# Performance work log

Hardware: AMD Instinct MI355X
Metric: run time of the kernel (lower is better)

Reference implementation:

```python
import jax, jax.numpy as jnp
import numpy as np

D_MODEL = 1024
N_HEADS = 16
D_HEAD = D_MODEL // N_HEADS
B, S = 2, 2048


def setup_inputs() -> dict:
    key = jax.random.key(0)
    ks = jax.random.split(key, 8)
    scale = 1.0 / np.sqrt(D_MODEL)
    return {
        "x": jax.random.normal(ks[0], (B, S, D_MODEL), dtype=jnp.float32),
        "Wq": jax.random.normal(ks[1], (D_MODEL, D_MODEL), dtype=jnp.float32) * scale,
        "bq": jnp.zeros((D_MODEL,), dtype=jnp.float32),
        "Wk": jax.random.normal(ks[2], (D_MODEL, D_MODEL), dtype=jnp.float32) * scale,
        "bk": jnp.zeros((D_MODEL,), dtype=jnp.float32),
        "Wv": jax.random.normal(ks[3], (D_MODEL, D_MODEL), dtype=jnp.float32) * scale,
        "bv": jnp.zeros((D_MODEL,), dtype=jnp.float32),
        "Wo": jax.random.normal(ks[4], (D_MODEL, D_MODEL), dtype=jnp.float32) * scale,
    }


def reference(x, Wq, bq, Wk, bk, Wv, bv, Wo):
    Bsz, Slen, D = x.shape
    # projections -> [B, H, S, Dh]
    def split_heads(t):
        return t.reshape(Bsz, Slen, N_HEADS, D_HEAD).transpose(0, 2, 1, 3)
    q = split_heads(x @ Wq + bq)
    k = split_heads(x @ Wk + bk)
    v = split_heads(x @ Wv + bv)
    scale = jnp.sqrt(jnp.float32(D_HEAD))
    scores = jnp.einsum('bhsd,bhtd->bhst', q, k) / scale  # [B,H,S,S]
    causal_mask = jnp.tril(jnp.ones((Slen, Slen), dtype=jnp.bool_))
    scores = jnp.where(causal_mask, scores, jnp.finfo(scores.dtype).min)
    attn = jax.nn.softmax(scores, axis=-1)
    # deterministic=True path: dropout is identity
    out = jnp.einsum('bhst,bhtd->bhsd', attn, v)
    out = out.transpose(0, 2, 1, 3).reshape(Bsz, Slen, D)
    return out @ Wo
```

## Files before the change

kernel.cpp:

```cpp
#include <hip/hip_runtime.h>
#include <hip/hip_bf16.h>

#define BATCH   2
#define SEQ     2048
#define DMODEL  1024
#define NHEADS  16
#define DHEAD   64
#define MROWS   (BATCH*SEQ)
#define NBH     (BATCH*NHEADS)

typedef float  f32x4  __attribute__((ext_vector_type(4)));
typedef short  s16x4  __attribute__((ext_vector_type(4)));
typedef short  s16x8  __attribute__((ext_vector_type(8)));
typedef __bf16 bf16x8 __attribute__((ext_vector_type(8)));

__device__ __forceinline__ short f2bf(float f) {
  union { float f; unsigned u; } v; v.f = f;
  return (short)((v.u + 0x7fffu + ((v.u >> 16) & 1u)) >> 16);
}
__device__ __forceinline__ float bf2f(short s) {
  union { unsigned u; float f; } v; v.u = ((unsigned)(unsigned short)s) << 16;
  return v.f;
}

__global__ void prep_fused(const float* __restrict__ x, short* __restrict__ xb,
                           const float* __restrict__ Wq, const float* __restrict__ Wk,
                           const float* __restrict__ Wv, const float* __restrict__ Wo,
                           short* __restrict__ WtQKV, short* __restrict__ WtO) {
  __shared__ float t[32][33];
  int z = blockIdx.z;
  int tx = threadIdx.x, ty = threadIdx.y;
  if (z >= 4) {
    int blk = (z - 4) * 1024 + blockIdx.y * 32 + blockIdx.x;
    int i = (blk * 256 + ty * 32 + tx) * 4;
    float4 v = *(const float4*)(x + i);
    s16x4 o = { f2bf(v.x), f2bf(v.y), f2bf(v.z), f2bf(v.w) };
    *(s16x4*)(xb + i) = o;
    return;
  }
  const float* W; short* Wt;
  if      (z == 0) { W = Wq; Wt = WtQKV; }
  else if (z == 1) { W = Wk; Wt = WtQKV + (1u << 20); }
  else if (z == 2) { W = Wv; Wt = WtQKV + (2u << 20); }
  else             { W = Wo; Wt = WtO; }
  int n0 = blockIdx.x * 32, k0 = blockIdx.y * 32;
  #pragma unroll
  for (int i = 0; i < 32; i += 8) t[ty + i][tx] = W[(k0 + ty + i) * DMODEL + n0 + tx];
  __syncthreads();
  #pragma unroll
  for (int i = 0; i < 32; i += 8) Wt[(n0 + ty + i) * DMODEL + k0 + tx] = f2bf(t[tx][ty + i]);
}

template<int MT, int NT, int EPI>
__global__ __launch_bounds__(256) void gemm_bf16(
    const short* __restrict__ A, const short* __restrict__ Bt,
    const float* __restrict__ bq, const float* __restrict__ bk, const float* __restrict__ bv,
    short* __restrict__ qb, short* __restrict__ kb, short* __restrict__ vt,
    float* __restrict__ out)
{
  constexpr int K = DMODEL, BK = 32;
  constexpr int WM = MT / 2, WN = NT / 2;
  constexpr int TM = WM / 16, TN = WN / 16;
  constexpr int CA = MT * BK / 512;
  constexpr int CB = NT * BK / 512;
  constexpr int SME = MT * BK + NT * BK;
  __shared__ short smem[SME];
  short* la = smem;
  short* lb = smem + MT * BK;
  const int tid = threadIdx.x;
  const int wave = tid >> 6, lane = tid & 63;
  const int quad = lane >> 4, l16 = lane & 15;
  const int wr = wave >> 1, wc = wave & 1;
  const int nx = gridDim.x, ny = gridDim.y;
  const int g = blockIdx.y * nx + blockIdx.x;
  const int xcd = g & 7, rr = g >> 3;
  const int m0 = (xcd * (ny >> 3) + rr / nx) * MT;
  const int n0 = (rr % nx) * NT;
  const int arow = lane >> 2, acol = (lane & 3) * 8;

  f32x4 acc[TM][TN] = {};

  for (int k0 = 0; k0 < K; k0 += BK) {
    for (int c = wave; c < CA; c += 4) {
      const short* gp = A + (m0 + c * 16 + arow) * K + k0 + acol;
      __builtin_amdgcn_global_load_lds((__attribute__((address_space(1))) void*)gp,
                                       (__attribute__((address_space(3))) void*)(la + c * 512),
                                       16, 0, 0);
    }
    for (int c = wave; c < CB; c += 4) {
      const short* gp = Bt + (n0 + c * 16 + arow) * K + k0 + acol;
      __builtin_amdgcn_global_load_lds((__attribute__((address_space(1))) void*)gp,
                                       (__attribute__((address_space(3))) void*)(lb + c * 512),
                                       16, 0, 0);
    }
    __syncthreads();
    bf16x8 af[TM], bfr[TN];
    #pragma unroll
    for (int i = 0; i < TM; ++i)
      af[i] = *(const bf16x8*)&la[(wr * WM + i * 16 + l16) * BK + quad * 8];
    #pragma unroll
    for (int j = 0; j < TN; ++j)
      bfr[j] = *(const bf16x8*)&lb[(wc * WN + j * 16 + l16) * BK + quad * 8];
    #pragma unroll
    for (int i = 0; i < TM; ++i)
      #pragma unroll
      for (int j = 0; j < TN; ++j)
        acc[i][j] = __builtin_amdgcn_mfma_f32_16x16x32_bf16(af[i], bfr[j], acc[i][j], 0, 0, 0);
    __syncthreads();
  }

  #pragma unroll
  for (int i = 0; i < TM; ++i)
    #pragma unroll
    for (int r = 0; r < 4; ++r) {
      int mrow = m0 + wr * WM + i * 16 + quad * 4 + r;
      #pragma unroll
      for (int j = 0; j < TN; ++j)
        out[mrow * DMODEL + n0 + wc * WN + j * 16 + l16] = acc[i][j][r];
    }
  (void)bq; (void)bk; (void)bv; (void)qb; (void)kb; (void)vt;
}

__global__ __launch_bounds__(512, 2) void gemm_qkv(
    const short* __restrict__ A, const short* __restrict__ Bt,
    const float* __restrict__ bq, const float* __restrict__ bk, const float* __restrict__ bv,
    short* __restrict__ qb, short* __restrict__ kb, short* __restrict__ vt)
{
  constexpr int K = DMODEL, BK = 64, NT = K / BK;
  __shared__ short lds[65536];
  const int tid = threadIdx.x;
  const int wave = tid >> 6, lane = tid & 63;
  const int quad = lane >> 4, l16 = lane & 15;
  const int wr = wave >> 2, wc = wave & 3;

  const int g  = blockIdx.x;
  const int s  = (g & 7) * 24 + (g >> 3);
  const int m0 = (s / 12) * 256, n0 = (s % 12) * 256;

  const int srow = lane >> 3;
  const int sgl  = (lane & 7) ^ srow;
  const short* gA = A  + (m0 + wave * 8 + srow) * K + sgl * 8;
  const short* gB = Bt + (n0 + wave * 8 + srow) * K + sgl * 8;

  auto stage = [&](int buf, int k0) {
    short* dA = lds + buf * 32768 + wave * 512;
    short* dB = dA + 16384;
    #pragma unroll
    for (int ss = 0; ss < 4; ++ss)
      __builtin_amdgcn_global_load_lds(
          (__attribute__((address_space(1))) void*)(gA + ss * 64 * K + k0),
          (__attribute__((address_space(3))) void*)(dA + ss * 4096), 16, 0, 0);
    #pragma unroll
    for (int ss = 0; ss < 4; ++ss)
      __builtin_amdgcn_global_load_lds(
          (__attribute__((address_space(1))) void*)(gB + ss * 64 * K + k0),
          (__attribute__((address_space(3))) void*)(dB + ss * 4096), 16, 0, 0);
  };

  const int swz = l16 & 7;
  f32x4 acc[8][4] = {};

  stage(0, 0);
  stage(1, BK);
  asm volatile("s_waitcnt vmcnt(0)" ::: "memory");
  __builtin_amdgcn_sched_barrier(0);
  __builtin_amdgcn_s_barrier();

  for (int t = 0; t < NT; ++t) {
    const int cur = t & 1;
    const short* bA = lds + cur * 32768;
    const short* bB = bA + 16384;

    bf16x8 a0[4], h0[4], b0[4];
    #pragma unroll
    for (int j = 0; j < 4; ++j)
      b0[j] = *(const bf16x8*)&bB[(wc * 64 + j * 16 + l16) * 64 + (quad ^ swz) * 8];
    #pragma unroll
    for (int i = 0; i < 4; ++i) {
      a0[i] = *(const bf16x8*)&bA[(wr * 128 + i * 16 + l16) * 64 + (quad ^ swz) * 8];
      h0[i] = *(const bf16x8*)&bA[(wr * 128 + 64 + i * 16 + l16) * 64 + (quad ^ swz) * 8];
    }
    __builtin_amdgcn_s_setprio(1);
    #pragma unroll
    for (int i = 0; i < 4; ++i)
      #pragma unroll
      for (int j = 0; j < 4; ++j) {
        acc[i][j]     = __builtin_amdgcn_mfma_f32_16x16x32_bf16(a0[i], b0[j], acc[i][j], 0, 0, 0);
        acc[4 + i][j] = __builtin_amdgcn_mfma_f32_16x16x32_bf16(h0[i], b0[j], acc[4 + i][j], 0, 0, 0);
      }
    __builtin_amdgcn_s_setprio(0);

    bf16x8 a1[4], h1[4], b1[4];
    #pragma unroll
    for (int j = 0; j < 4; ++j)
      b1[j] = *(const bf16x8*)&bB[(wc * 64 + j * 16 + l16) * 64 + ((4 | quad) ^ swz) * 8];
    #pragma unroll
    for (int i = 0; i < 4; ++i) {
      a1[i] = *(const bf16x8*)&bA[(wr * 128 + i * 16 + l16) * 64 + ((4 | quad) ^ swz) * 8];
      h1[i] = *(const bf16x8*)&bA[(wr * 128 + 64 + i * 16 + l16) * 64 + ((4 | quad) ^ swz) * 8];
    }
    asm volatile("s_waitcnt lgkmcnt(0)" ::: "memory");
    __builtin_amdgcn_sched_barrier(0);
    __builtin_amdgcn_s_barrier();
    if (t + 2 < NT) stage(cur, (t + 2) * BK);

    __builtin_amdgcn_s_setprio(1);
    #pragma unroll
    for (int i = 0; i < 4; ++i)
      #pragma unroll
      for (int j = 0; j < 4; ++j) {
        acc[i][j]     = __builtin_amdgcn_mfma_f32_16x16x32_bf16(a1[i], b1[j], acc[i][j], 0, 0, 0);
        acc[4 + i][j] = __builtin_amdgcn_mfma_f32_16x16x32_bf16(h1[i], b1[j], acc[4 + i][j], 0, 0, 0);
      }
    __builtin_amdgcn_s_setprio(0);

    if (t + 1 < NT) {
      if (t + 2 < NT) asm volatile("s_waitcnt vmcnt(8)" ::: "memory");
      else            asm volatile("s_waitcnt vmcnt(0)" ::: "memory");
      __builtin_amdgcn_sched_barrier(0);
      __builtin_amdgcn_s_barrier();
    }
  }

  const int b = m0 >> 11, s0 = m0 & (SEQ - 1);
  const int sel = n0 >> 10;
  const int n0rel = n0 & (DMODEL - 1);
  const float* bias = (sel == 0) ? bq : (sel == 1) ? bk : bv;
  const float scl = (sel == 0) ? 0.125f * 1.44269504089f : 1.0f;
  const bool isV = (sel == 2);
  short* eT = lds;

  __syncthreads();
  for (int hp = 0; hp < 2; ++hp) {
    if ((wc >> 1) == hp) {
      #pragma unroll
      for (int j = 0; j < 4; ++j) {
        int coll = wc * 64 + j * 16 + l16;
        int cl = coll & 127;
        float bias_v = bias[n0rel + coll];
        #pragma unroll
        for (int i = 0; i < 8; ++i) {
          int rowb = wr * 128 + i * 16 + quad * 4;
          #pragma unroll
          for (int r = 0; r < 4; ++r) {
            short val = f2bf((acc[i][j][r] + bias_v) * scl);
            if (isV) eT[cl * 264 + rowb + r] = val;
            else     eT[(rowb + r) * 136 + cl] = val;
          }
        }
      }
    }
    __syncthreads();
    if (!isV) {
      short* dst = (sel == 0) ? qb : kb;
      const int rseg = tid & 15, rrow = tid >> 4;
      #pragma unroll
      for (int it = 0; it < 8; ++it) {
        int row = it * 32 + rrow;
        int colg = n0rel + hp * 128 + rseg * 8;
        int h = colg >> 6, d = colg & 63;
        s16x8 v = *(const s16x8*)&eT[row * 136 + rseg * 8];
        *(s16x8*)(dst + ((b * NHEADS + h) * SEQ + s0 + row) * DHEAD + d) = v;
      }
    } else {
      const int sseg = tid & 31, dl0 = tid >> 5;
      #pragma unroll
      for (int it = 0; it < 8; ++it) {
        int dloc = it * 16 + dl0;
        int colg = n0rel + hp * 128 + dloc;
        int h = colg >> 6, d = colg & 63;
        s16x8 v = *(const s16x8*)&eT[dloc * 264 + sseg * 8];
        *(s16x8*)(vt + ((b * NHEADS + h) * DHEAD + d) * SEQ + s0 + sseg * 8) = v;
      }
    }
    __syncthreads();
  }
}

__global__ __launch_bounds__(256, 2) void attn_k(
    const short* __restrict__ qbp, const short* __restrict__ kbp,
    const short* __restrict__ vtb, short* __restrict__ oP, float* __restrict__ lP)
{
  __shared__ short kls[2][8192];
  __shared__ short vls[2][8192];
  const int tid = threadIdx.x, wave = tid >> 6, lane = tid & 63;
  const int quad = lane >> 4, l16 = lane & 15;
  const int hi = blockIdx.x >> 8;
  const int q6 = (blockIdx.x >> 6) & 3;
  const int qg = hi ? 7 - q6 : q6;
  const int half = (blockIdx.x >> 5) & 1;
  const int bh = blockIdx.x & 31;
  const int qt1 = qg * 8 + wave * 2;
  const int mF[4] = { qt1 * 16, (qt1 + 1) * 16, (126 - qt1) * 16, (127 - qt1) * 16 };
  const int nch = (127 - 8 * qg) / 4 + 1;
  const short* Q  = qbp + bh * SEQ * DHEAD;
  const short* Kp = kbp + bh * SEQ * DHEAD;
  const short* Vt = vtb + bh * DHEAD * SEQ;

  bf16x8 qf[4][2];
  #pragma unroll
  for (int f = 0; f < 4; ++f) {
    qf[f][0] = *(const bf16x8*)&Q[(mF[f] + l16) * DHEAD + quad * 8];
    qf[f][1] = *(const bf16x8*)&Q[(mF[f] + l16) * DHEAD + 32 + quad * 8];
  }

  float lF[4] = {};
  f32x4 oF[4][4] = {};

  const int vdl = lane >> 3, vsl = lane & 7;

  auto stage1 = [&](int buf, int slot, int t0) {
    #pragma unroll
    for (int j = 0; j < 2; ++j) {
      int g = j * 4 + wave;
      const short* gp = Kp + (t0 + lane) * DHEAD + g * 8;
      __builtin_amdgcn_global_load_lds((__attribute__((address_space(1))) void*)gp,
                                       (__attribute__((address_space(3))) void*)&kls[buf][slot * 4096 + g * 512],
                                       16, 0, 0);
    }
    #pragma unroll
    for (int j = 0; j < 2; ++j) {
      int gd = j * 4 + wave;
      const short* gp = Vt + (gd * 8 + vdl) * SEQ + t0 + ((vsl ^ vdl) * 8);
      __builtin_amdgcn_global_load_lds((__attribute__((address_space(1))) void*)gp,
                                       (__attribute__((address_space(3))) void*)&vls[buf][slot * 4096 + gd * 512],
                                       16, 0, 0);
    }
  };
  auto stagepair = [&](int buf, int cc) {
    stage1(buf, 0, cc * 64);
    if (cc + 2 < nch) stage1(buf, 1, (cc + 2) * 64);
  };

  stagepair(0, half);
  int it = 0;
  for (int cc = half; cc < nch; cc += 4, ++it) {
    __syncthreads();
    if (cc + 4 < nch) stagepair((it + 1) & 1, cc + 4);
    const int buf = it & 1;
    #pragma unroll
    for (int u = 0; u < 2; ++u) {
      const int c = cc + 2 * u;
      if (c < nch) {
        const int t0 = c * 64;
        const int sb = u * 4096;
        #pragma unroll
        for (int t = 0; t < 4; ++t) {
          const int tb = t0 + t * 16;
          if (tb <= mF[3]) {
            bf16x8 kf0 = *(const bf16x8*)&kls[buf][sb + ((0 + quad) * 64 + t * 16 + l16) * 8];
            bf16x8 kf1 = *(const bf16x8*)&kls[buf][sb + ((4 + quad) * 64 + t * 16 + l16) * 8];
            s16x4 vf[4];
            {
              int gsw = ((t * 2 + (quad >> 1)) ^ (l16 & 7));
              #pragma unroll
              for (int dt = 0; dt < 4; ++dt)
                vf[dt] = *(const s16x4*)&vls[buf][sb + ((dt * 16 + l16) * 8 + gsw) * 8 + (quad & 1) * 4];
            }
            #pragma unroll
            for (int f = 0; f < 4; ++f) {
              if (tb <= mF[f]) {
                f32x4 a = {};
                a = __builtin_amdgcn_mfma_f32_16x16x32_bf16(kf0, qf[f][0], a, 0, 0, 0);
                a = __builtin_amdgcn_mfma_f32_16x16x32_bf16(kf1, qf[f][1], a, 0, 0, 0);
                if (tb == mF[f]) {
                  #pragma unroll
                  for (int r = 0; r < 4; ++r)
                    if (quad * 4 + r > l16) a[r] = -1e30f;
                }
                f32x4 p;
                #pragma unroll
                for (int r = 0; r < 4; ++r) p[r] = __builtin_amdgcn_exp2f(a[r]);
                lF[f] += (p[0] + p[1]) + (p[2] + p[3]);
                __hip_bfloat162 c01 = __float22bfloat162_rn(float2{p[0], p[1]});
                __hip_bfloat162 c23 = __float22bfloat162_rn(float2{p[2], p[3]});
                union { unsigned u2[2]; s16x4 s; } pu;
                pu.u2[0] = *(unsigned*)&c01; pu.u2[1] = *(unsigned*)&c23;
                #pragma unroll
                for (int dt = 0; dt < 4; ++dt)
                  oF[f][dt] = __builtin_amdgcn_mfma_f32_16x16x16bf16_1k(pu.s, vf[dt], oF[f][dt], 0, 0, 0);
              }
            }
          }
        }
      }
    }
  }

  float* lD = lP + (half * NBH + bh) * SEQ;
  short* oD = oP + ((half * NBH + bh) * SEQ) * DHEAD;
  #pragma unroll
  for (int f = 0; f < 4; ++f) {
    float l = lF[f];
    l += __shfl_xor(l, 16, 64); l += __shfl_xor(l, 32, 64);
    if (quad == 0) lD[mF[f] + l16] = l;
    #pragma unroll
    for (int r = 0; r < 4; ++r) {
      int s = mF[f] + quad * 4 + r;
      #pragma unroll
      for (int dt = 0; dt < 4; ++dt)
        oD[s * DHEAD + dt * 16 + l16] = f2bf(oF[f][dt][r]);
    }
  }
}

__global__ void attn_merge(const short* __restrict__ oP, const float* __restrict__ lP,
                           short* __restrict__ ob) {
  int idx = blockIdx.x * 256 + threadIdx.x;
  int d8 = idx & 7, s = (idx >> 3) & (SEQ - 1), bh = idx >> 14;
  s16x8 e = *(const s16x8*)&oP[((0   + bh) * SEQ + s) * DHEAD + d8 * 8];
  s16x8 o = *(const s16x8*)&oP[((NBH + bh) * SEQ + s) * DHEAD + d8 * 8];
  float linv = 1.0f / (lP[bh * SEQ + s] + lP[(NBH + bh) * SEQ + s]);
  s16x8 r;
  #pragma unroll
  for (int k = 0; k < 8; ++k) r[k] = f2bf((bf2f(e[k]) + bf2f(o[k])) * linv);
  int b = bh >> 4, h = bh & 15;
  *(s16x8*)&ob[(b * SEQ + s) * DMODEL + h * DHEAD + d8 * 8] = r;
}

extern "C" void kernel_launch(void* const* d_in, const int* in_sizes, int n_in,
                              void* d_out, int out_size, void* d_ws, size_t ws_size,
                              hipStream_t stream) {
  const float* x  = (const float*)d_in[0];
  const float* Wq = (const float*)d_in[1];
  const float* bq = (const float*)d_in[2];
  const float* Wk = (const float*)d_in[3];
  const float* bk = (const float*)d_in[4];
  const float* Wv = (const float*)d_in[5];
  const float* bv = (const float*)d_in[6];
  const float* Wo = (const float*)d_in[7];
  float* out = (float*)d_out;

  char* ws = (char*)d_ws;
  short* xb  = (short*)(ws);
  short* wtq = (short*)(ws + (8u  << 20));
  short* wto = (short*)(ws + (14u << 20));
  short* qb  = (short*)(ws + (16u << 20));
  short* kb  = (short*)(ws + (24u << 20));
  short* vt  = (short*)(ws + (32u << 20));
  short* ob  = (short*)(ws + (40u << 20));
  short* oP  = (short*)(ws + (48u << 20));
  float* lP  = (float*)(ws + (80u << 20));

  prep_fused<<<dim3(32, 32, 8), dim3(32, 8), 0, stream>>>(x, xb, Wq, Wk, Wv, Wo, wtq, wto);

  gemm_qkv<<<dim3(192), 512, 0, stream>>>(xb, wtq, bq, bk, bv, qb, kb, vt);

  attn_k<<<8 * NBH * 2, 256, 0, stream>>>(qb, kb, vt, oP, lP);
  attn_merge<<<NBH * SEQ * 8 / 256, 256, 0, stream>>>(oP, lP, ob);

  gemm_bf16<64, 128, 1><<<dim3(DMODEL / 128, MROWS / 64), 256, 0, stream>>>(
      ob, wto, nullptr, nullptr, nullptr, nullptr, nullptr, nullptr, out);
}
```

Measured before the change: 189.1 us.

## Restructure QKV GEMM main loop into four-phase half-tile pipelined schedule

Rewrites the QKV projection GEMM's k-loop so the A and B tiles are staged in half-tiles, with loads interleaved across four MFMA phases per iteration, in the style of an 8-wave ping-pong schedule. The aim is finer-grained overlap of global-to-LDS loads with matrix math, and a smaller register footprint because only one A fragment set is live at a time. In exchange it adds more workgroup barriers per iteration and relies on tricky vmcnt accounting, so it is sensitive to correctness and scheduling.

Measured after the change: 191.2 us. Within noise of the previous version (+1.1%).

```diff
diff --git a/kernel.cpp b/kernel.cpp
--- a/kernel.cpp
+++ b/kernel.cpp
@@ -139,88 +139,92 @@
 
   const int srow = lane >> 3;
   const int sgl  = (lane & 7) ^ srow;
-  const short* gA = A  + (m0 + wave * 8 + srow) * K + sgl * 8;
-  const short* gB = Bt + (n0 + wave * 8 + srow) * K + sgl * 8;
-
-  auto stage = [&](int buf, int k0) {
-    short* dA = lds + buf * 32768 + wave * 512;
-    short* dB = dA + 16384;
-    #pragma unroll
-    for (int ss = 0; ss < 4; ++ss)
+  const short* gA0 = A  + (m0 + wave * 16 + srow) * K + sgl * 8;
+  const short* gB0 = Bt + (n0 + wave * 16 + srow) * K + sgl * 8;
+
+  auto stageA = [&](int par, int half, int k0) {
+    short* d = lds + (par * 2 + half) * 8192 + wave * 1024;
+    #pragma unroll
+    for (int ss = 0; ss < 2; ++ss)
       __builtin_amdgcn_global_load_lds(
-          (__attribute__((address_space(1))) void*)(gA + ss * 64 * K + k0),
-          (__attribute__((address_space(3))) void*)(dA + ss * 4096), 16, 0, 0);
-    #pragma unroll
-    for (int ss = 0; ss < 4; ++ss)
+          (__attribute__((address_space(1))) void*)(gA0 + (half * 128 + ss * 8) * K + k0),
+          (__attribute__((address_space(3))) void*)(d + ss * 512), 16, 0, 0);
+  };
+  auto stageB = [&](int par, int half, int k0) {
+    short* d = lds + 32768 + (par * 2 + half) * 8192 + wave * 1024;
+    #pragma unroll
+    for (int ss = 0; ss < 2; ++ss)
       __builtin_amdgcn_global_load_lds(
-          (__attribute__((address_space(1))) void*)(gB + ss * 64 * K + k0),
-          (__attribute__((address_space(3))) void*)(dB + ss * 4096), 16, 0, 0);
+          (__attribute__((address_space(1))) void*)(gB0 + (half * 128 + ss * 8) * K + k0),
+          (__attribute__((address_space(3))) void*)(d + ss * 512), 16, 0, 0);
   };
 
   const int swz = l16 & 7;
   f32x4 acc[8][4] = {};
 
-  stage(0, 0);
-  stage(1, BK);
-  asm volatile("s_waitcnt vmcnt(0)" ::: "memory");
-  __builtin_amdgcn_sched_barrier(0);
-  __builtin_amdgcn_s_barrier();
+  auto readA = [&](bf16x8* a, int par, int mh, int kh) {
+    const short* sl = lds + (par * 2 + wr) * 8192;
+    #pragma unroll
+    for (int i = 0; i < 4; ++i)
+      a[i] = *(const bf16x8*)&sl[(mh * 64 + i * 16 + l16) * 64 + (((kh << 2) | quad) ^ swz) * 8];
+  };
+  auto readB = [&](bf16x8* bf, int par, int kh) {
+    const short* sl = lds + 32768 + (par * 2 + (wc >> 1)) * 8192;
+    #pragma unroll
+    for (int j = 0; j < 4; ++j)
+      bf[j] = *(const bf16x8*)&sl[((wc & 1) * 64 + j * 16 + l16) * 64 + (((kh << 2) | quad) ^ swz) * 8];
+  };
+  auto mfma16 = [&](int mh, bf16x8* a, bf16x8* bf) {
+    #pragma unroll
+    for (int i = 0; i < 4; ++i)
+      #pragma unroll
+      for (int j = 0; j < 4; ++j)
+        acc[mh * 4 + i][j] = __builtin_amdgcn_mfma_f32_16x16x32_bf16(a[i], bf[j], acc[mh * 4 + i][j], 0, 0, 0);
+  };
+
+#define QBAR()  __builtin_amdgcn_s_barrier()
+#define QSBAR() __builtin_amdgcn_sched_barrier(0)
+#define QLGKM() { asm volatile("s_waitcnt lgkmcnt(0)" ::: "memory"); QSBAR(); }
+
+  stageA(0, 0, 0); stageA(0, 1, 0); stageB(0, 0, 0); stageB(0, 1, 0);
+  stageB(1, 0, BK);
+  asm volatile("s_waitcnt vmcnt(2)" ::: "memory"); QSBAR();
+  QBAR(); QSBAR();
 
   for (int t = 0; t < NT; ++t) {
-    const int cur = t & 1;
-    const short* bA = lds + cur * 32768;
-    const short* bB = bA + 16384;
-
-    bf16x8 a0[4], h0[4], b0[4];
-    #pragma unroll
-    for (int j = 0; j < 4; ++j)
-      b0[j] = *(const bf16x8*)&bB[(wc * 64 + j * 16 + l16) * 64 + (quad ^ swz) * 8];
-    #pragma unroll
-    for (int i = 0; i < 4; ++i) {
-      a0[i] = *(const bf16x8*)&bA[(wr * 128 + i * 16 + l16) * 64 + (quad ^ swz) * 8];
-      h0[i] = *(const bf16x8*)&bA[(wr * 128 + 64 + i * 16 + l16) * 64 + (quad ^ swz) * 8];
-    }
-    __builtin_amdgcn_s_setprio(1);
-    #pragma unroll
-    for (int i = 0; i < 4; ++i)
-      #pragma unroll
-      for (int j = 0; j < 4; ++j) {
-        acc[i][j]     = __builtin_amdgcn_mfma_f32_16x16x32_bf16(a0[i], b0[j], acc[i][j], 0, 0, 0);
-        acc[4 + i][j] = __builtin_amdgcn_mfma_f32_16x16x32_bf16(h0[i], b0[j], acc[4 + i][j], 0, 0, 0);
-      }
-    __builtin_amdgcn_s_setprio(0);
-
-    bf16x8 a1[4], h1[4], b1[4];
-    #pragma unroll
-    for (int j = 0; j < 4; ++j)
-      b1[j] = *(const bf16x8*)&bB[(wc * 64 + j * 16 + l16) * 64 + ((4 | quad) ^ swz) * 8];
-    #pragma unroll
-    for (int i = 0; i < 4; ++i) {
-      a1[i] = *(const bf16x8*)&bA[(wr * 128 + i * 16 + l16) * 64 + ((4 | quad) ^ swz) * 8];
-      h1[i] = *(const bf16x8*)&bA[(wr * 128 + 64 + i * 16 + l16) * 64 + ((4 | quad) ^ swz) * 8];
-    }
-    asm volatile("s_waitcnt lgkmcnt(0)" ::: "memory");
-    __builtin_amdgcn_sched_barrier(0);
-    __builtin_amdgcn_s_barrier();
-    if (t + 2 < NT) stage(cur, (t + 2) * BK);
-
-    __builtin_amdgcn_s_setprio(1);
-    #pragma unroll
-    for (int i = 0; i < 4; ++i)
-      #pragma unroll
-      for (int j = 0; j < 4; ++j) {
-        acc[i][j]     = __builtin_amdgcn_mfma_f32_16x16x32_bf16(a1[i], b1[j], acc[i][j], 0, 0, 0);
-        acc[4 + i][j] = __builtin_amdgcn_mfma_f32_16x16x32_bf16(h1[i], b1[j], acc[4 + i][j], 0, 0, 0);
-      }
-    __builtin_amdgcn_s_setprio(0);
-
-    if (t + 1 < NT) {
-      if (t + 2 < NT) asm volatile("s_waitcnt vmcnt(8)" ::: "memory");
-      else            asm volatile("s_waitcnt vmcnt(0)" ::: "memory");
-      __builtin_amdgcn_sched_barrier(0);
-      __builtin_amdgcn_s_barrier();
-    }
-  }
+    const int par = t & 1, nxt = par ^ 1;
+    const int kn = (t + 1) * BK;
+    bf16x8 aF[4], bF[4];
+
+    readB(bF, par, 0); readA(aF, par, 0, 0);
+    if (t + 1 < NT) stageB(nxt, 1, kn);
+    QBAR(); QLGKM();
+    __builtin_amdgcn_s_setprio(1); mfma16(0, aF, bF); __builtin_amdgcn_s_setprio(0);
+    QBAR(); QSBAR();
+
+    readA(aF, par, 1, 0);
+    if (t + 1 < NT) stageA(nxt, 0, kn);
+    QBAR(); QLGKM();
+    __builtin_amdgcn_s_setprio(1); mfma16(1, aF, bF); __builtin_amdgcn_s_setprio(0);
+    QBAR(); QSBAR();
+
+    readB(bF, par, 1); readA(aF, par, 0, 1);
+    if (t + 1 < NT) stageA(nxt, 1, kn);
+    QBAR(); QLGKM();
+    __builtin_amdgcn_s_setprio(1); mfma16(0, aF, bF); __builtin_amdgcn_s_setprio(0);
+    QBAR(); QSBAR();
+
+    readA(aF, par, 1, 1);
+    if (t + 2 < NT) stageB(par, 0, (t + 2) * BK);
+    QBAR(); QLGKM();
+    __builtin_amdgcn_s_setprio(1); mfma16(1, aF, bF); __builtin_amdgcn_s_setprio(0);
+    if (t + 2 < NT)      { asm volatile("s_waitcnt vmcnt(2)" ::: "memory"); QSBAR(); }
+    else if (t + 1 < NT) { asm volatile("s_waitcnt vmcnt(0)" ::: "memory"); QSBAR(); }
+    QBAR(); QSBAR();
+  }
+#undef QBAR
+#undef QSBAR
+#undef QLGKM
 
   const int b = m0 >> 11, s0 = m0 & (SEQ - 1);
   const int sel = n0 >> 10;
```
